# Kernel optimization log

Hardware: AMD Instinct MI355X
Metric: run time of the kernel (lower is better)

## Reference

```python
import jax, jax.numpy as jnp
import numpy as np

NEIGH_W = 0.25  # self.neigh_w
act = jax.nn.leaky_relu  # negative_slope=0.01, matches nn.LeakyReLU default


def _lin(x, w, b):
    # torch Linear with weight stored as [in, out]
    return x @ w + b


def setup_inputs() -> dict:
    key = jax.random.key(0)
    I, C, L = 1024, 32, 64  # images, curves/image, points/curve (uniform segments)
    N = I * C * L
    ks = jax.random.split(key, 32)

    def p(k, shape, scale=0.1):
        return jax.random.normal(k, shape, dtype=jnp.float32) * scale

    curve_tensor = jax.random.normal(ks[0], (N, 8), dtype=jnp.float32)
    # segment-boundary labels: col1 = curve start (every L rows), col0 = image start (every L*C rows)
    lab = np.zeros((N, 2), np.int64)
    lab[::L, 1] = 1
    lab[::L * C, 0] = 1
    curve_label = jnp.asarray(lab)
    cors_batch = jax.random.normal(ks[1], (I, C, C, 5), dtype=jnp.float32)

    inp = dict(curve_tensor=curve_tensor, curve_label=curve_label, cors_batch=cors_batch)
    dims = [("crv_mlp", 8, 8), ("crv_lv1", 24, 32), ("crv_lv2", 32, 24),
            ("inter1", 24, 24), ("inter2", 24, 24),
            ("grp1", 72, 24), ("grp2", 24, 24), ("grp3", 24, 24),
            ("img1", 24, 18), ("img2", 18, 12), ("img3", 12, 6)]
    for i, (name, din, dout) in enumerate(dims):
        inp[name + "_w"] = p(ks[2 + 2 * i], (din, dout))
        inp[name + "_b"] = p(ks[3 + 2 * i], (dout,))
    # cor_mlp is initialized to all ones (cor_init_rand=0 in the original)
    inp["cor_w"] = jnp.ones((5, 24), jnp.float32)
    inp["cor_b"] = jnp.ones((24,), jnp.float32)
    return inp


def reference(curve_tensor, curve_label, cors_batch,
              crv_mlp_w, crv_mlp_b, crv_lv1_w, crv_lv1_b, crv_lv2_w, crv_lv2_b,
              inter1_w, inter1_b, inter2_w, inter2_b, cor_w, cor_b,
              grp1_w, grp1_b, grp2_w, grp2_b, grp3_w, grp3_b,
              img1_w, img1_b, img2_w, img2_b, img3_w, img3_b):
    I, C = cors_batch.shape[0], cors_batch.shape[1]
    L = curve_tensor.shape[0] // (I * C)

    # ---- curve level: ring-graph roll aggregation within each curve segment ----
    x = curve_tensor.reshape(I * C, L, 8)

    def agg(t):
        neigh = _lin(jnp.roll(t, 1, axis=1), crv_mlp_w, crv_mlp_b) \
              + _lin(jnp.roll(t, -1, axis=1), crv_mlp_w, crv_mlp_b)
        return NEIGH_W * neigh + (1.0 - 2.0 * NEIGH_W) * t

    x1 = agg(x)
    x2 = agg(x1)
    embed = jnp.concatenate([x, x1, x2], axis=-1)            # [I*C, L, 24]
    feat = act(_lin(act(_lin(embed, crv_lv1_w, crv_lv1_b)), crv_lv2_w, crv_lv2_b))
    group = feat.mean(axis=1)                                 # [I*C, 24] per-curve feature
    group = act(_lin(act(_lin(group, inter1_w, inter1_b)), inter2_w, inter2_b))

    # ---- image level: pairwise cor-weighted aggregation over curves per image ----
    g = group.reshape(I, C, 24)
    cor = act(_lin(cors_batch, cor_w, cor_b))                 # [I, C, C, 24]

    def cagg(t):
        # after[i,j,d] = sum_k before[i,k,d] * cor[i,j,k,d]
        return jnp.einsum('ikd,ijkd->ijd', t, cor)

    g1 = cagg(g)
    g2 = cagg(g1)
    emb = jnp.concatenate([g, g1, g2], axis=-1)               # [I, C, 72]
    h = act(_lin(act(_lin(act(_lin(emb, grp1_w, grp1_b)), grp2_w, grp2_b)), grp3_w, grp3_b))
    img = h.mean(axis=1)                                      # [I, 24]

    out = _lin(act(_lin(act(_lin(img, img1_w, img1_b)), img2_w, img2_b)), img3_w, img3_b)
    return jax.nn.sigmoid(out)                                # [I, brands]
```

## Files before the change

### kernel.cpp

```cpp
#include <hip/hip_runtime.h>
#include <hip/hip_bf16.h>
#include <math.h>

#define LEAKY(x) fmaxf((x), 0.01f * (x))

typedef float v2f __attribute__((ext_vector_type(2)));
typedef __bf16 bf8 __attribute__((ext_vector_type(8)));
typedef float f4 __attribute__((ext_vector_type(4)));

constexpr int IMGS = 1024;
constexpr int CRV  = 32;
constexpr int LPT  = 64;

__device__ __forceinline__ void ldseg(float* dst, const float* __restrict__ src,
                                      int n, int tid, int nt) {
  for (int i = tid; i < n; i += nt) dst[i] = src[i];
}

__device__ __forceinline__ v2f pk_leaky(v2f x) {
  return __builtin_elementwise_max(x, x * 0.01f);
}
__device__ __forceinline__ f4 leaky4(f4 x) {
  return __builtin_elementwise_max(x, x * 0.01f);
}

__device__ __forceinline__ float ring_sum(float v) {
  int s = __builtin_bit_cast(int, v);
  int a = __builtin_amdgcn_update_dpp(0, s, 0x134, 0xF, 0xF, false);
  int b = __builtin_amdgcn_update_dpp(0, s, 0x13C, 0xF, 0xF, false);
  return __builtin_bit_cast(float, a) + __builtin_bit_cast(float, b);
}

__device__ __forceinline__ unsigned bfpair(float x, float y) {
  __hip_bfloat162 h = __float22bfloat162_rn(make_float2(x, y));
  unsigned r;
  __builtin_memcpy(&r, &h, 4);
  return r;
}

#define WOFF(pp, cc) (((pp) << 4) + ((((cc) + ((pp) >> 1)) & 3) << 2))

__global__ __launch_bounds__(256) void curve_kernel(
    const float* __restrict__ ct,
    const float* __restrict__ mw,  const float* __restrict__ mb,
    const float* __restrict__ w1,  const float* __restrict__ b1,
    const float* __restrict__ w2,  const float* __restrict__ b2,
    const float* __restrict__ i1w, const float* __restrict__ i1b,
    const float* __restrict__ i2w, const float* __restrict__ i2b,
    float* __restrict__ gout)
{
  __shared__ __align__(16) unsigned sW1t[512];
  __shared__ __align__(16) unsigned sW2t[512];
  __shared__ __align__(16) float    sB2[32];
  __shared__ __align__(16) unsigned sX[4][1024];
  __shared__ __align__(16) float    srow[4][32];

  const int tid  = threadIdx.x;
  const int wave = tid >> 6;
  const int lane = tid & 63;
  const int curve = blockIdx.x * 4 + wave;

  for (int idx = tid; idx < 512; idx += 256) {
    int n  = idx >> 4;
    int kp = idx & 15;
    int k0 = kp * 2;
    int word = (n << 4) + ((((kp >> 2) + (n >> 1)) & 3) << 2) + (kp & 3);
    float a0 = (k0 < 24) ? w1[k0 * 32 + n] : ((k0 == 24) ? b1[n] : 0.0f);
    float a1 = (k0 + 1 < 24) ? w1[(k0 + 1) * 32 + n] : 0.0f;
    sW1t[word] = bfpair(a0, a1);
    float c0 = (n < 24) ? w2[k0 * 24 + n] : 0.0f;
    float c1 = (n < 24) ? w2[(k0 + 1) * 24 + n] : 0.0f;
    sW2t[word] = bfpair(c0, c1);
  }
  if (tid < 32) sB2[tid] = (tid < 24) ? b2[tid] : 0.0f;
  __syncthreads();

  const float* p = ct + ((size_t)curve * LPT + lane) * 8;
  float e[24];
  float4 t0 = *(const float4*)p;
  float4 t1 = *(const float4*)(p + 4);
  e[0] = t0.x; e[1] = t0.y; e[2] = t0.z; e[3] = t0.w;
  e[4] = t1.x; e[5] = t1.y; e[6] = t1.z; e[7] = t1.w;

  {
    v2f y[4];
    #pragma unroll
    for (int j = 0; j < 4; j++) y[j] = *(const v2f*)&mb[2 * j];
    #pragma unroll
    for (int i = 0; i < 8; i++) {
      v2f ev = (v2f){e[i], e[i]};
      #pragma unroll
      for (int j = 0; j < 4; j++)
        y[j] = __builtin_elementwise_fma(ev, *(const v2f*)&mw[i * 8 + 2 * j], y[j]);
    }
    #pragma unroll
    for (int j = 0; j < 4; j++) {
      float n0 = ring_sum(y[j].x);
      float n1 = ring_sum(y[j].y);
      e[8 + 2 * j]     = 0.25f * n0 + 0.5f * e[2 * j];
      e[8 + 2 * j + 1] = 0.25f * n1 + 0.5f * e[2 * j + 1];
    }
  }
  {
    v2f y[4];
    #pragma unroll
    for (int j = 0; j < 4; j++) y[j] = *(const v2f*)&mb[2 * j];
    #pragma unroll
    for (int i = 0; i < 8; i++) {
      v2f ev = (v2f){e[8 + i], e[8 + i]};
      #pragma unroll
      for (int j = 0; j < 4; j++)
        y[j] = __builtin_elementwise_fma(ev, *(const v2f*)&mw[i * 8 + 2 * j], y[j]);
    }
    #pragma unroll
    for (int j = 0; j < 4; j++) {
      float n0 = ring_sum(y[j].x);
      float n1 = ring_sum(y[j].y);
      e[16 + 2 * j]     = 0.25f * n0 + 0.5f * e[8 + 2 * j];
      e[16 + 2 * j + 1] = 0.25f * n1 + 0.5f * e[8 + 2 * j + 1];
    }
  }

  unsigned* Xw = &sX[wave][0];
  {
    uint4 wv;
    wv.x = bfpair(e[0], e[1]);  wv.y = bfpair(e[2], e[3]);
    wv.z = bfpair(e[4], e[5]);  wv.w = bfpair(e[6], e[7]);
    *(uint4*)&Xw[WOFF(lane, 0)] = wv;
    wv.x = bfpair(e[8], e[9]);  wv.y = bfpair(e[10], e[11]);
    wv.z = bfpair(e[12], e[13]); wv.w = bfpair(e[14], e[15]);
    *(uint4*)&Xw[WOFF(lane, 1)] = wv;
    wv.x = bfpair(e[16], e[17]); wv.y = bfpair(e[18], e[19]);
    wv.z = bfpair(e[20], e[21]); wv.w = bfpair(e[22], e[23]);
    *(uint4*)&Xw[WOFF(lane, 2)] = wv;
    wv.x = 0x00003f80u; wv.y = 0u; wv.z = 0u; wv.w = 0u;
    *(uint4*)&Xw[WOFF(lane, 3)] = wv;
  }
  __builtin_amdgcn_wave_barrier();

  const int q   = lane >> 4;
  const int c16 = lane & 15;

  f4 d[2][4];
  {
    bf8 aw[2], bx[4];
    #pragma unroll
    for (int mt = 0; mt < 2; mt++)
      aw[mt] = __builtin_bit_cast(bf8, *(const uint4*)&sW1t[WOFF(c16 + mt * 16, q)]);
    #pragma unroll
    for (int nt = 0; nt < 4; nt++)
      bx[nt] = __builtin_bit_cast(bf8, *(const uint4*)&Xw[WOFF(c16 + nt * 16, q)]);
    const f4 z = (f4){0.f, 0.f, 0.f, 0.f};
    #pragma unroll
    for (int mt = 0; mt < 2; mt++)
      #pragma unroll
      for (int nt = 0; nt < 4; nt++)
        d[mt][nt] = __builtin_amdgcn_mfma_f32_16x16x32_bf16(aw[mt], bx[nt], z, 0, 0, 0);
  }
  #pragma unroll
  for (int mt = 0; mt < 2; mt++) {
    #pragma unroll
    for (int nt = 0; nt < 4; nt++) {
      f4 v = leaky4(d[mt][nt]);
      const int prow = nt * 16 + c16;
      const int word = WOFF(prow, mt * 2 + (q >> 1)) + (q & 1) * 2;
      uint2 pk; pk.x = bfpair(v.x, v.y); pk.y = bfpair(v.z, v.w);
      *(uint2*)&Xw[word] = pk;
    }
  }
  __builtin_amdgcn_wave_barrier();

  f4 d2[2][4];
  {
    bf8 a2[2], bh[4];
    #pragma unroll
    for (int mt = 0; mt < 2; mt++)
      a2[mt] = __builtin_bit_cast(bf8, *(const uint4*)&sW2t[WOFF(c16 + mt * 16, q)]);
    #pragma unroll
    for (int nt = 0; nt < 4; nt++)
      bh[nt] = __builtin_bit_cast(bf8, *(const uint4*)&Xw[WOFF(c16 + nt * 16, q)]);
    f4 cb_[2];
    #pragma unroll
    for (int mt = 0; mt < 2; mt++)
      cb_[mt] = *(const f4*)&sB2[mt * 16 + q * 4];
    #pragma unroll
    for (int mt = 0; mt < 2; mt++)
      #pragma unroll
      for (int nt = 0; nt < 4; nt++)
        d2[mt][nt] = __builtin_amdgcn_mfma_f32_16x16x32_bf16(a2[mt], bh[nt], cb_[mt], 0, 0, 0);
  }

  float m8[2][4];
  #pragma unroll
  for (int mt = 0; mt < 2; mt++) {
    f4 t = leaky4(d2[mt][0]) + leaky4(d2[mt][1]);
    t = t + leaky4(d2[mt][2]);
    t = t + leaky4(d2[mt][3]);
    #pragma unroll
    for (int r = 0; r < 4; r++) {
      float s = t[r];
      s += __shfl_xor(s, 1);
      s += __shfl_xor(s, 2);
      s += __shfl_xor(s, 4);
      s += __shfl_xor(s, 8);
      m8[mt][r] = s * (1.0f / 64.0f);
    }
  }
  if (c16 == 0) {
    f4 v0 = (f4){m8[0][0], m8[0][1], m8[0][2], m8[0][3]};
    *(f4*)&srow[wave][q * 4] = v0;
    if (q < 2) {
      f4 v1 = (f4){m8[1][0], m8[1][1], m8[1][2], m8[1][3]};
      *(f4*)&srow[wave][16 + q * 4] = v1;
    }
  }
  __builtin_amdgcn_wave_barrier();

  float sv[24];
  #pragma unroll
  for (int i = 0; i < 24; i++) sv[i] = srow[wave][i];

  const int jd = (lane < 24) ? lane : 0;
  float a = i1b[jd];
  #pragma unroll
  for (int i = 0; i < 24; i++) a += sv[i] * i1w[i * 24 + jd];
  a = LEAKY(a);
  if (lane < 24) srow[wave][lane] = a;
  __builtin_amdgcn_wave_barrier();

  float av[24];
  #pragma unroll
  for (int i = 0; i < 24; i++) av[i] = srow[wave][i];

  float o = i2b[jd];
  #pragma unroll
  for (int i = 0; i < 24; i++) o += av[i] * i2w[i * 24 + jd];
  o = LEAKY(o);

  if (lane < 24) gout[(size_t)curve * 24 + lane] = o;
}

__global__ __launch_bounds__(768) void image_kernel(
    const float* __restrict__ cors, const float* __restrict__ gin,
    const float* __restrict__ cw,  const float* __restrict__ cb,
    const float* __restrict__ g1w, const float* __restrict__ g1b,
    const float* __restrict__ g2w, const float* __restrict__ g2b,
    const float* __restrict__ g3w, const float* __restrict__ g3b,
    const float* __restrict__ m1w, const float* __restrict__ m1b,
    const float* __restrict__ m2w, const float* __restrict__ m2b,
    const float* __restrict__ m3w, const float* __restrict__ m3b,
    float* __restrict__ out)
{
  __shared__ __align__(16) float sCorsP[CRV * CRV * 8];
  __shared__ __align__(16) float sG0[CRV * 24], sG1[CRV * 24], sG2[CRV * 24];
  __shared__ __align__(16) float sHa[CRV * 24], sHb[CRV * 24];
  __shared__ float sW1[1728], sW2[576], sW3[576];
  __shared__ float sT[96];

  const int tid = threadIdx.x;
  const int img = blockIdx.x;
  const int j = tid / 24;
  const int d = tid - j * 24;

  {
    const float* cbase = cors + (size_t)img * (CRV * CRV * 5);
    for (int idx = tid; idx < CRV * CRV * 5; idx += 768) {
      int jj = idx / 160;
      int r  = idx - jj * 160;
      int k  = r / 5;
      int c  = r - k * 5;
      sCorsP[(jj * CRV + k) * 8 + c] = cbase[idx];
    }
  }
  sG0[tid] = gin[(size_t)img * (CRV * 24) + tid];
  ldseg(sW1, g1w, 1728, tid, 768);
  ldseg(sW2, g2w, 576, tid, 768);
  ldseg(sW3, g3w, 576, tid, 768);
  float wc0 = cw[0 * 24 + d], wc1 = cw[1 * 24 + d], wc2 = cw[2 * 24 + d];
  float wc3 = cw[3 * 24 + d], wc4 = cw[4 * 24 + d];
  float cbd = cb[d];
  float g1bd = g1b[d], g2bd = g2b[d], g3bd = g3b[d];
  __syncthreads();

  float corv[CRV];
  #pragma unroll
  for (int k = 0; k < CRV; k++) {
    const float* cr = &sCorsP[(j * CRV + k) * 8];
    float4 qq = *(const float4*)cr;
    float q4 = cr[4];
    float v = cbd + qq.x * wc0 + qq.y * wc1 + qq.z * wc2 + qq.w * wc3 + q4 * wc4;
    corv[k] = LEAKY(v);
  }
  {
    float t1 = 0.0f;
    #pragma unroll
    for (int k = 0; k < CRV; k++) t1 += sG0[k * 24 + d] * corv[k];
    sG1[j * 24 + d] = t1;
  }
  __syncthreads();
  {
    float t2 = 0.0f;
    #pragma unroll
    for (int k = 0; k < CRV; k++) t2 += sG1[k * 24 + d] * corv[k];
    sG2[j * 24 + d] = t2;
  }
  __syncthreads();
  {
    float v = g1bd;
    #pragma unroll
    for (int i = 0; i < 24; i++) v += sG0[j * 24 + i] * sW1[i * 24 + d];
    #pragma unroll
    for (int i = 0; i < 24; i++) v += sG1[j * 24 + i] * sW1[(24 + i) * 24 + d];
    #pragma unroll
    for (int i = 0; i < 24; i++) v += sG2[j * 24 + i] * sW1[(48 + i) * 24 + d];
    sHa[j * 24 + d] = LEAKY(v);
  }
  __syncthreads();
  {
    float v = g2bd;
    #pragma unroll
    for (int i = 0; i < 24; i++) v += sHa[j * 24 + i] * sW2[i * 24 + d];
    sHb[j * 24 + d] = LEAKY(v);
  }
  __syncthreads();
  {
    float v = g3bd;
    #pragma unroll
    for (int i = 0; i < 24; i++) v += sHb[j * 24 + i] * sW3[i * 24 + d];
    sHa[j * 24 + d] = LEAKY(v);
  }
  __syncthreads();
  if (tid < 24) {
    float s = 0.0f;
    #pragma unroll
    for (int k = 0; k < CRV; k++) s += sHa[k * 24 + tid];
    sT[tid] = s * (1.0f / CRV);
  }
  __syncthreads();
  if (tid < 18) {
    float v = m1b[tid];
    #pragma unroll
    for (int i = 0; i < 24; i++) v += sT[i] * m1w[i * 18 + tid];
    sT[32 + tid] = LEAKY(v);
  }
  __syncthreads();
  if (tid < 12) {
    float v = m2b[tid];
    #pragma unroll
    for (int i = 0; i < 18; i++) v += sT[32 + i] * m2w[i * 12 + tid];
    sT[56 + tid] = LEAKY(v);
  }
  __syncthreads();
  if (tid < 6) {
    float v = m3b[tid];
    #pragma unroll
    for (int i = 0; i < 12; i++) v += sT[56 + i] * m3w[i * 6 + tid];
    out[img * 6 + tid] = 1.0f / (1.0f + expf(-v));
  }
}

extern "C" void kernel_launch(void* const* d_in, const int* in_sizes, int n_in,
                              void* d_out, int out_size, void* d_ws, size_t ws_size,
                              hipStream_t stream) {
  const float* ct   = (const float*)d_in[0];
  const float* cors = (const float*)d_in[2];
  const float* mw  = (const float*)d_in[3];
  const float* mb  = (const float*)d_in[4];
  const float* w1  = (const float*)d_in[5];
  const float* b1  = (const float*)d_in[6];
  const float* w2  = (const float*)d_in[7];
  const float* b2  = (const float*)d_in[8];
  const float* i1w = (const float*)d_in[9];
  const float* i1b = (const float*)d_in[10];
  const float* i2w = (const float*)d_in[11];
  const float* i2b = (const float*)d_in[12];

  const float *cw, *cb, *g1w, *g1b, *g2w, *g2b, *g3w, *g3b;
  const float *m1w, *m1b, *m2w, *m2b, *m3w, *m3b;
  if (in_sizes[13] == 120) {
    cw  = (const float*)d_in[13]; cb  = (const float*)d_in[14];
    g1w = (const float*)d_in[15]; g1b = (const float*)d_in[16];
    g2w = (const float*)d_in[17]; g2b = (const float*)d_in[18];
    g3w = (const float*)d_in[19]; g3b = (const float*)d_in[20];
    m1w = (const float*)d_in[21]; m1b = (const float*)d_in[22];
    m2w = (const float*)d_in[23]; m2b = (const float*)d_in[24];
    m3w = (const float*)d_in[25]; m3b = (const float*)d_in[26];
  } else {
    g1w = (const float*)d_in[13]; g1b = (const float*)d_in[14];
    g2w = (const float*)d_in[15]; g2b = (const float*)d_in[16];
    g3w = (const float*)d_in[17]; g3b = (const float*)d_in[18];
    m1w = (const float*)d_in[19]; m1b = (const float*)d_in[20];
    m2w = (const float*)d_in[21]; m2b = (const float*)d_in[22];
    m3w = (const float*)d_in[23]; m3b = (const float*)d_in[24];
    cw  = (const float*)d_in[25]; cb  = (const float*)d_in[26];
  }

  float* group = (float*)d_ws;
  float* out = (float*)d_out;

  curve_kernel<<<(IMGS * CRV) / 4, 256, 0, stream>>>(
      ct, mw, mb, w1, b1, w2, b2, i1w, i1b, i2w, i2b, group);
  image_kernel<<<IMGS, 768, 0, stream>>>(
      cors, group, cw, cb, g1w, g1b, g2w, g2b, g3w, g3b,
      m1w, m1b, m2w, m2b, m3w, m3b, out);
}
```

Baseline: 231.1 us.

## Fold ring aggregation into first-layer weights via a one-block prep kernel

Because the curve-level neighbour aggregation is linear, the embedding matmul is rewritten in terms of x, ring_sum(x) and ring_sum(ring_sum(x)). The per-curve 8x8 mixes are folded into an effective W1 and bias, which a new single-block prep kernel computes on each call. That prep kernel also pre-packs the MFMA A-fragments and the bias C-fragments, and stores transposed inter-layer weights. The curve kernel then loads these directly into registers instead of building LDS weight tables with a block-wide sync in every block, and it uses float4 loads for the inter MLP. The cost is an extra kernel launch, a serialized one-block prep step, and slightly different bf16 rounding of the folded weights.

```diff
diff --git a/kernel.cpp b/kernel.cpp
--- a/kernel.cpp
+++ b/kernel.cpp
@@ -17,9 +17,6 @@
   for (int i = tid; i < n; i += nt) dst[i] = src[i];
 }
 
-__device__ __forceinline__ v2f pk_leaky(v2f x) {
-  return __builtin_elementwise_max(x, x * 0.01f);
-}
 __device__ __forceinline__ f4 leaky4(f4 x) {
   return __builtin_elementwise_max(x, x * 0.01f);
 }
@@ -40,18 +37,82 @@
 
 #define WOFF(pp, cc) (((pp) << 4) + ((((cc) + ((pp) >> 1)) & 3) << 2))
 
+__device__ float w1eff_val(const float* mw, const float* mb,
+                           const float* w1, const float* b1, int n, int k) {
+  if (k < 8) {
+    return w1[k * 32 + n] + 0.5f * w1[(8 + k) * 32 + n] + 0.25f * w1[(16 + k) * 32 + n];
+  } else if (k < 16) {
+    int a = k - 8;
+    float s = 0.f;
+    for (int i = 0; i < 8; i++)
+      s += mw[a * 8 + i] * (w1[(8 + i) * 32 + n] + w1[(16 + i) * 32 + n]);
+    return 0.25f * s;
+  } else if (k < 24) {
+    int a = k - 16;
+    float s = 0.f;
+    for (int i = 0; i < 8; i++) {
+      float m2 = 0.f;
+      for (int c = 0; c < 8; c++) m2 += mw[a * 8 + c] * mw[c * 8 + i];
+      s += m2 * w1[(16 + i) * 32 + n];
+    }
+    return 0.0625f * s;
+  } else if (k == 24) {
+    float s = b1[n];
+    for (int i = 0; i < 8; i++) {
+      s += mb[i] * (0.5f * w1[(8 + i) * 32 + n] + 0.75f * w1[(16 + i) * 32 + n]);
+      float wb = 0.f;
+      for (int c = 0; c < 8; c++) wb += mb[c] * mw[c * 8 + i];
+      s += 0.25f * wb * w1[(16 + i) * 32 + n];
+    }
+    return s;
+  }
+  return 0.f;
+}
+
+__global__ __launch_bounds__(256) void prep_kernel(
+    const float* __restrict__ mw, const float* __restrict__ mb,
+    const float* __restrict__ w1, const float* __restrict__ b1,
+    const float* __restrict__ w2, const float* __restrict__ b2,
+    const float* __restrict__ i1w, const float* __restrict__ i2w,
+    unsigned* __restrict__ fragA1, unsigned* __restrict__ fragA2,
+    float* __restrict__ fragC,
+    float* __restrict__ i1wT, float* __restrict__ i2wT)
+{
+  const int tid = threadIdx.x;
+  for (int idx = tid; idx < 512; idx += 256) {
+    int tile = idx >> 8;
+    int lane = (idx >> 2) & 63;
+    int word = idx & 3;
+    int n  = tile * 16 + (lane & 15);
+    int k0 = (lane >> 4) * 8 + word * 2;
+    fragA1[idx] = bfpair(w1eff_val(mw, mb, w1, b1, n, k0),
+                         w1eff_val(mw, mb, w1, b1, n, k0 + 1));
+    float u0 = (n < 24) ? w2[k0 * 24 + n] : 0.f;
+    float u1 = (n < 24) ? w2[(k0 + 1) * 24 + n] : 0.f;
+    fragA2[idx] = bfpair(u0, u1);
+  }
+  for (int idx = tid; idx < 512; idx += 256) {
+    int tile = idx >> 8;
+    int lane = (idx >> 2) & 63;
+    int r = idx & 3;
+    int n = tile * 16 + ((lane >> 4) & 3) * 4 + r;
+    fragC[idx] = (n < 24) ? b2[n] : 0.f;
+  }
+  for (int idx = tid; idx < 576; idx += 256) {
+    int jj = idx / 24, ii = idx - jj * 24;
+    i1wT[idx] = i1w[ii * 24 + jj];
+    i2wT[idx] = i2w[ii * 24 + jj];
+  }
+}
+
 __global__ __launch_bounds__(256) void curve_kernel(
     const float* __restrict__ ct,
-    const float* __restrict__ mw,  const float* __restrict__ mb,
-    const float* __restrict__ w1,  const float* __restrict__ b1,
-    const float* __restrict__ w2,  const float* __restrict__ b2,
-    const float* __restrict__ i1w, const float* __restrict__ i1b,
-    const float* __restrict__ i2w, const float* __restrict__ i2b,
+    const unsigned* __restrict__ fragA1, const unsigned* __restrict__ fragA2,
+    const float* __restrict__ fragC,
+    const float* __restrict__ i1wT, const float* __restrict__ i1b,
+    const float* __restrict__ i2wT, const float* __restrict__ i2b,
     float* __restrict__ gout)
 {
-  __shared__ __align__(16) unsigned sW1t[512];
-  __shared__ __align__(16) unsigned sW2t[512];
-  __shared__ __align__(16) float    sB2[32];
   __shared__ __align__(16) unsigned sX[4][1024];
   __shared__ __align__(16) float    srow[4][32];
 
@@ -60,78 +121,38 @@
   const int lane = tid & 63;
   const int curve = blockIdx.x * 4 + wave;
 
-  for (int idx = tid; idx < 512; idx += 256) {
-    int n  = idx >> 4;
-    int kp = idx & 15;
-    int k0 = kp * 2;
-    int word = (n << 4) + ((((kp >> 2) + (n >> 1)) & 3) << 2) + (kp & 3);
-    float a0 = (k0 < 24) ? w1[k0 * 32 + n] : ((k0 == 24) ? b1[n] : 0.0f);
-    float a1 = (k0 + 1 < 24) ? w1[(k0 + 1) * 32 + n] : 0.0f;
-    sW1t[word] = bfpair(a0, a1);
-    float c0 = (n < 24) ? w2[k0 * 24 + n] : 0.0f;
-    float c1 = (n < 24) ? w2[(k0 + 1) * 24 + n] : 0.0f;
-    sW2t[word] = bfpair(c0, c1);
-  }
-  if (tid < 32) sB2[tid] = (tid < 24) ? b2[tid] : 0.0f;
-  __syncthreads();
+  uint4 awv[2], a2v[2];
+  float4 cbv[2];
+  #pragma unroll
+  for (int mt = 0; mt < 2; mt++) {
+    awv[mt] = *(const uint4*)(fragA1 + mt * 256 + lane * 4);
+    a2v[mt] = *(const uint4*)(fragA2 + mt * 256 + lane * 4);
+    cbv[mt] = *(const float4*)(fragC + mt * 256 + lane * 4);
+  }
 
   const float* p = ct + ((size_t)curve * LPT + lane) * 8;
-  float e[24];
   float4 t0 = *(const float4*)p;
   float4 t1 = *(const float4*)(p + 4);
-  e[0] = t0.x; e[1] = t0.y; e[2] = t0.z; e[3] = t0.w;
-  e[4] = t1.x; e[5] = t1.y; e[6] = t1.z; e[7] = t1.w;
-
-  {
-    v2f y[4];
-    #pragma unroll
-    for (int j = 0; j < 4; j++) y[j] = *(const v2f*)&mb[2 * j];
-    #pragma unroll
-    for (int i = 0; i < 8; i++) {
-      v2f ev = (v2f){e[i], e[i]};
-      #pragma unroll
-      for (int j = 0; j < 4; j++)
-        y[j] = __builtin_elementwise_fma(ev, *(const v2f*)&mw[i * 8 + 2 * j], y[j]);
-    }
-    #pragma unroll
-    for (int j = 0; j < 4; j++) {
-      float n0 = ring_sum(y[j].x);
-      float n1 = ring_sum(y[j].y);
-      e[8 + 2 * j]     = 0.25f * n0 + 0.5f * e[2 * j];
-      e[8 + 2 * j + 1] = 0.25f * n1 + 0.5f * e[2 * j + 1];
-    }
-  }
-  {
-    v2f y[4];
-    #pragma unroll
-    for (int j = 0; j < 4; j++) y[j] = *(const v2f*)&mb[2 * j];
-    #pragma unroll
-    for (int i = 0; i < 8; i++) {
-      v2f ev = (v2f){e[8 + i], e[8 + i]};
-      #pragma unroll
-      for (int j = 0; j < 4; j++)
-        y[j] = __builtin_elementwise_fma(ev, *(const v2f*)&mw[i * 8 + 2 * j], y[j]);
-    }
-    #pragma unroll
-    for (int j = 0; j < 4; j++) {
-      float n0 = ring_sum(y[j].x);
-      float n1 = ring_sum(y[j].y);
-      e[16 + 2 * j]     = 0.25f * n0 + 0.5f * e[8 + 2 * j];
-      e[16 + 2 * j + 1] = 0.25f * n1 + 0.5f * e[8 + 2 * j + 1];
-    }
-  }
+  float x[8];
+  x[0] = t0.x; x[1] = t0.y; x[2] = t0.z; x[3] = t0.w;
+  x[4] = t1.x; x[5] = t1.y; x[6] = t1.z; x[7] = t1.w;
+  float s1[8], t2[8];
+  #pragma unroll
+  for (int i = 0; i < 8; i++) s1[i] = ring_sum(x[i]);
+  #pragma unroll
+  for (int i = 0; i < 8; i++) t2[i] = ring_sum(s1[i]);
 
   unsigned* Xw = &sX[wave][0];
   {
     uint4 wv;
-    wv.x = bfpair(e[0], e[1]);  wv.y = bfpair(e[2], e[3]);
-    wv.z = bfpair(e[4], e[5]);  wv.w = bfpair(e[6], e[7]);
+    wv.x = bfpair(x[0], x[1]);  wv.y = bfpair(x[2], x[3]);
+    wv.z = bfpair(x[4], x[5]);  wv.w = bfpair(x[6], x[7]);
     *(uint4*)&Xw[WOFF(lane, 0)] = wv;
-    wv.x = bfpair(e[8], e[9]);  wv.y = bfpair(e[10], e[11]);
-    wv.z = bfpair(e[12], e[13]); wv.w = bfpair(e[14], e[15]);
+    wv.x = bfpair(s1[0], s1[1]); wv.y = bfpair(s1[2], s1[3]);
+    wv.z = bfpair(s1[4], s1[5]); wv.w = bfpair(s1[6], s1[7]);
     *(uint4*)&Xw[WOFF(lane, 1)] = wv;
-    wv.x = bfpair(e[16], e[17]); wv.y = bfpair(e[18], e[19]);
-    wv.z = bfpair(e[20], e[21]); wv.w = bfpair(e[22], e[23]);
+    wv.x = bfpair(t2[0], t2[1]); wv.y = bfpair(t2[2], t2[3]);
+    wv.z = bfpair(t2[4], t2[5]); wv.w = bfpair(t2[6], t2[7]);
     *(uint4*)&Xw[WOFF(lane, 2)] = wv;
     wv.x = 0x00003f80u; wv.y = 0u; wv.z = 0u; wv.w = 0u;
     *(uint4*)&Xw[WOFF(lane, 3)] = wv;
@@ -143,19 +164,18 @@
 
   f4 d[2][4];
   {
-    bf8 aw[2], bx[4];
-    #pragma unroll
-    for (int mt = 0; mt < 2; mt++)
-      aw[mt] = __builtin_bit_cast(bf8, *(const uint4*)&sW1t[WOFF(c16 + mt * 16, q)]);
+    bf8 bx[4];
     #pragma unroll
     for (int nt = 0; nt < 4; nt++)
       bx[nt] = __builtin_bit_cast(bf8, *(const uint4*)&Xw[WOFF(c16 + nt * 16, q)]);
     const f4 z = (f4){0.f, 0.f, 0.f, 0.f};
     #pragma unroll
-    for (int mt = 0; mt < 2; mt++)
+    for (int mt = 0; mt < 2; mt++) {
+      bf8 aw = __builtin_bit_cast(bf8, awv[mt]);
       #pragma unroll
       for (int nt = 0; nt < 4; nt++)
-        d[mt][nt] = __builtin_amdgcn_mfma_f32_16x16x32_bf16(aw[mt], bx[nt], z, 0, 0, 0);
+        d[mt][nt] = __builtin_amdgcn_mfma_f32_16x16x32_bf16(aw, bx[nt], z, 0, 0, 0);
+    }
   }
   #pragma unroll
   for (int mt = 0; mt < 2; mt++) {
@@ -172,22 +192,18 @@
 
   f4 d2[2][4];
   {
-    bf8 a2[2], bh[4];
-    #pragma unroll
-    for (int mt = 0; mt < 2; mt++)
-      a2[mt] = __builtin_bit_cast(bf8, *(const uint4*)&sW2t[WOFF(c16 + mt * 16, q)]);
+    bf8 bh[4];
     #pragma unroll
     for (int nt = 0; nt < 4; nt++)
       bh[nt] = __builtin_bit_cast(bf8, *(const uint4*)&Xw[WOFF(c16 + nt * 16, q)]);
-    f4 cb_[2];
-    #pragma unroll
-    for (int mt = 0; mt < 2; mt++)
-      cb_[mt] = *(const f4*)&sB2[mt * 16 + q * 4];
-    #pragma unroll
-    for (int mt = 0; mt < 2; mt++)
+    #pragma unroll
+    for (int mt = 0; mt < 2; mt++) {
+      bf8 a2 = __builtin_bit_cast(bf8, a2v[mt]);
+      f4 cb_ = __builtin_bit_cast(f4, cbv[mt]);
       #pragma unroll
       for (int nt = 0; nt < 4; nt++)
-        d2[mt][nt] = __builtin_amdgcn_mfma_f32_16x16x32_bf16(a2[mt], bh[nt], cb_[mt], 0, 0, 0);
+        d2[mt][nt] = __builtin_amdgcn_mfma_f32_16x16x32_bf16(a2, bh[nt], cb_, 0, 0, 0);
+    }
   }
 
   float m8[2][4];
@@ -223,7 +239,11 @@
   const int jd = (lane < 24) ? lane : 0;
   float a = i1b[jd];
   #pragma unroll
-  for (int i = 0; i < 24; i++) a += sv[i] * i1w[i * 24 + jd];
+  for (int t = 0; t < 6; t++) {
+    float4 wv = *(const float4*)&i1wT[jd * 24 + t * 4];
+    a += sv[t * 4 + 0] * wv.x + sv[t * 4 + 1] * wv.y
+       + sv[t * 4 + 2] * wv.z + sv[t * 4 + 3] * wv.w;
+  }
   a = LEAKY(a);
   if (lane < 24) srow[wave][lane] = a;
   __builtin_amdgcn_wave_barrier();
@@ -234,7 +254,11 @@
 
   float o = i2b[jd];
   #pragma unroll
-  for (int i = 0; i < 24; i++) o += av[i] * i2w[i * 24 + jd];
+  for (int t = 0; t < 6; t++) {
+    float4 wv = *(const float4*)&i2wT[jd * 24 + t * 4];
+    o += av[t * 4 + 0] * wv.x + av[t * 4 + 1] * wv.y
+       + av[t * 4 + 2] * wv.z + av[t * 4 + 3] * wv.w;
+  }
   o = LEAKY(o);
 
   if (lane < 24) gout[(size_t)curve * 24 + lane] = o;
@@ -395,11 +419,20 @@
     cw  = (const float*)d_in[25]; cb  = (const float*)d_in[26];
   }
 
-  float* group = (float*)d_ws;
+  float* wsf = (float*)d_ws;
+  float* group = wsf;
+  const size_t base = (size_t)IMGS * CRV * 24;
+  unsigned* fragA1 = (unsigned*)(wsf + base);
+  unsigned* fragA2 = fragA1 + 512;
+  float*    fragC  = (float*)(fragA2 + 512);
+  float*    i1wT   = fragC + 512;
+  float*    i2wT   = i1wT + 576;
   float* out = (float*)d_out;
 
+  prep_kernel<<<1, 256, 0, stream>>>(mw, mb, w1, b1, w2, b2, i1w, i2w,
+                                     fragA1, fragA2, fragC, i1wT, i2wT);
   curve_kernel<<<(IMGS * CRV) / 4, 256, 0, stream>>>(
-      ct, mw, mb, w1, b1, w2, b2, i1w, i1b, i2w, i2b, group);
+      ct, fragA1, fragA2, fragC, i1wT, i1b, i2wT, i2b, group);
   image_kernel<<<IMGS, 768, 0, stream>>>(
       cors, group, cw, cb, g1w, g1b, g2w, g2b, g3w, g3b,
       m1w, m1b, m2w, m2b, m3w, m3b, out);
```

After: 227.0 us. Within noise of the previous version (-1.8%).
